# Performance work log

Measured on AMD Instinct MI355X. Metric: run time of the kernel, lower is better.

The kernel has to match this reference:

```python
import jax, jax.numpy as jnp
import numpy as np

N = 8192
IN_DIM = 64
OUT_DIM = 64
HEADS = 2
EPS = 1e-10


def setup_inputs() -> dict:
    key = jax.random.key(0)
    ks = jax.random.split(key, 6)
    features = jax.random.normal(ks[0], (N, IN_DIM), dtype=jnp.float32)
    adj = (jax.random.uniform(ks[1], (N, N)) < 0.005).astype(jnp.float32)
    # per-head attention linear: Linear(2*in_dim, 1) stacked -> [heads, 2*in_dim]
    W_attn = jax.random.normal(ks[2], (HEADS, 2 * IN_DIM), dtype=jnp.float32) * 0.05
    b_attn = jax.random.normal(ks[3], (HEADS,), dtype=jnp.float32) * 0.05
    # feature transform: Linear(in_dim, heads*out_dim)
    W_lin = jax.random.normal(ks[4], (HEADS * OUT_DIM, IN_DIM), dtype=jnp.float32) * 0.05
    b_lin = jax.random.normal(ks[5], (HEADS * OUT_DIM,), dtype=jnp.float32) * 0.05
    return {"adj": adj, "features": features, "W_attn": W_attn,
            "b_attn": b_attn, "W_lin": W_lin, "b_lin": b_lin}


def reference(adj, features, W_attn, b_attn, W_lin, b_lin):
    n, in_dim = features.shape
    heads = W_attn.shape[0]
    # add self-loops (adj + sparse identity in the original)
    idx = jnp.arange(n)
    adj_sl = adj.at[idx, idx].add(1.0)
    # concat-based score: head([x_i ; x_j]) = x_i @ Wa_src + x_j @ Wa_dst + b
    # (avoids the O(N^2 * 2*in_dim) concat tensor the original materializes)
    s_src = features @ W_attn[:, :in_dim].T   # [N, H]
    s_dst = features @ W_attn[:, in_dim:].T   # [N, H]
    # scores[n,h,m] = exp(s_src[n,h] + s_dst[m,h] + b[h])
    scores = jnp.exp(s_src[:, :, None] + s_dst.T[None, :, :] + b_attn[None, :, None])
    scores = scores * adj_sl[:, None, :]                      # adjacency mask
    attn = scores / (jnp.sum(scores, axis=-1, keepdims=True) + EPS)
    # dropout is identity in eval mode (deterministic reference)
    ft = (features @ W_lin.T + b_lin).reshape(n, heads, -1)   # [N, H, OUT]
    out = jnp.einsum('nhm,mhj->nhj', attn, ft)                # aggregate neighbors
    return jax.nn.elu(out.reshape(n, -1))
```

## Files before the change

kernel.cpp:

```cpp
#include <hip/hip_runtime.h>
#include <math.h>

#define NN 8192
#define IN_DIM 64
#define GAT_EPS 1e-10f
#define ECAP 256

typedef float fvec4 __attribute__((ext_vector_type(4)));

__device__ __forceinline__ unsigned nz4(fvec4 v) {
    return (unsigned)(v.x != 0.f) | ((unsigned)(v.y != 0.f) << 1) |
           ((unsigned)(v.z != 0.f) << 2) | ((unsigned)(v.w != 0.f) << 3);
}

__global__ void setup_kernel(const float* __restrict__ features,
                             const float* __restrict__ W_lin,
                             const float* __restrict__ b_lin,
                             const float* __restrict__ W_attn,
                             float2* __restrict__ ftI,
                             float2* __restrict__ pdv) {
    if (blockIdx.x < 2048) {
        int gid = blockIdx.x * blockDim.x + threadIdx.x;
        int n = gid >> 6;
        int c = gid & 63;
        const float4* f4 = (const float4*)(features + (size_t)n * IN_DIM);
        const float4* w0 = (const float4*)(W_lin + (size_t)c * IN_DIM);
        const float4* w1 = (const float4*)(W_lin + (size_t)(64 + c) * IN_DIM);
        float a0 = 0.f, a1 = 0.f;
#pragma unroll
        for (int d = 0; d < IN_DIM / 4; ++d) {
            float4 f = f4[d];
            float4 u = w0[d];
            float4 v = w1[d];
            a0 += f.x * u.x + f.y * u.y + f.z * u.z + f.w * u.w;
            a1 += f.x * v.x + f.y * v.y + f.z * v.z + f.w * v.w;
        }
        ftI[gid] = make_float2(a0 + b_lin[c], a1 + b_lin[64 + c]);
    } else {
        int n = (blockIdx.x - 2048) * blockDim.x + threadIdx.x;
        const float4* f4   = (const float4*)(features + (size_t)n * IN_DIM);
        const float4* wa0d = (const float4*)(W_attn + IN_DIM);
        const float4* wa1d = (const float4*)(W_attn + 3 * IN_DIM);
        float s0 = 0.f, s1 = 0.f;
#pragma unroll
        for (int d = 0; d < IN_DIM / 4; ++d) {
            float4 f = f4[d];
            float4 b = wa0d[d];
            float4 e = wa1d[d];
            s0 += f.x * b.x + f.y * b.y + f.z * b.z + f.w * b.w;
            s1 += f.x * e.x + f.y * e.y + f.z * e.z + f.w * e.w;
        }
        pdv[n] = make_float2(__expf(s0), __expf(s1));
    }
}

__global__ void __launch_bounds__(256) gat_agg_kernel(
        const float* __restrict__ adj,
        const float2* __restrict__ ftI,
        const float2* __restrict__ pdv,
        float* __restrict__ out) {
    __shared__ int edges[4][ECAP];
    __shared__ int ecnt[4];
    int widx = threadIdx.x >> 6;
    int lane = threadIdx.x & 63;
    int n = blockIdx.x * 4 + widx;
    int* ebuf = edges[widx];

    if (lane == 0) ecnt[widx] = 0;

    const fvec4* arow = (const fvec4*)(adj + (size_t)n * NN) + lane;

    fvec4 q[3][4];
#pragma unroll
    for (int r = 0; r < 3; ++r) {
        const fvec4* p = arow + r * 256;
        q[r][0] = __builtin_nontemporal_load(p);
        q[r][1] = __builtin_nontemporal_load(p + 64);
        q[r][2] = __builtin_nontemporal_load(p + 128);
        q[r][3] = __builtin_nontemporal_load(p + 192);
    }

#pragma unroll
    for (int it = 0; it < 8; ++it) {
        int slot = it % 3;
        fvec4 a0 = q[slot][0], a1 = q[slot][1], a2 = q[slot][2], a3 = q[slot][3];
        if (it < 5) {
            const fvec4* p = arow + (it + 3) * 256;
            q[slot][0] = __builtin_nontemporal_load(p);
            q[slot][1] = __builtin_nontemporal_load(p + 64);
            q[slot][2] = __builtin_nontemporal_load(p + 128);
            q[slot][3] = __builtin_nontemporal_load(p + 192);
        }
        unsigned mb = nz4(a0) | (nz4(a1) << 4) | (nz4(a2) << 8) | (nz4(a3) << 12);
        if (mb) {
            int c = __popc(mb);
            int pos = atomicAdd(&ecnt[widx], c);
            int megabase = it * 1024 + lane * 4;
            while (mb) {
                int b = __ffs(mb) - 1;
                mb &= mb - 1;
                ebuf[pos++] = megabase + ((b >> 2) << 8) + (b & 3);
            }
        }
    }

    float2 ps = pdv[n];
    float2 fs = ftI[(size_t)n * 64 + lane];
    float acc0 = ps.x * fs.x, acc1 = ps.y * fs.y;
    float den0 = ps.x, den1 = ps.y;

    __syncthreads();

    int count = ecnt[widx];
    int e = 0;
    for (; e + 8 <= count; e += 8) {
        int4 ma  = *(const int4*)&ebuf[e];
        int4 mbq = *(const int4*)&ebuf[e + 4];
        float2 p0 = pdv[ma.x],  p1 = pdv[ma.y],  p2 = pdv[ma.z],  p3 = pdv[ma.w];
        float2 p4 = pdv[mbq.x], p5 = pdv[mbq.y], p6 = pdv[mbq.z], p7 = pdv[mbq.w];
        float2 f0 = ftI[(size_t)ma.x * 64 + lane];
        float2 f1 = ftI[(size_t)ma.y * 64 + lane];
        float2 f2 = ftI[(size_t)ma.z * 64 + lane];
        float2 f3 = ftI[(size_t)ma.w * 64 + lane];
        float2 f4 = ftI[(size_t)mbq.x * 64 + lane];
        float2 f5 = ftI[(size_t)mbq.y * 64 + lane];
        float2 f6 = ftI[(size_t)mbq.z * 64 + lane];
        float2 f7 = ftI[(size_t)mbq.w * 64 + lane];
        acc0 += p0.x * f0.x + p1.x * f1.x + p2.x * f2.x + p3.x * f3.x
              + p4.x * f4.x + p5.x * f5.x + p6.x * f6.x + p7.x * f7.x;
        acc1 += p0.y * f0.y + p1.y * f1.y + p2.y * f2.y + p3.y * f3.y
              + p4.y * f4.y + p5.y * f5.y + p6.y * f6.y + p7.y * f7.y;
        den0 += p0.x + p1.x + p2.x + p3.x + p4.x + p5.x + p6.x + p7.x;
        den1 += p0.y + p1.y + p2.y + p3.y + p4.y + p5.y + p6.y + p7.y;
    }
    for (; e < count; ++e) {
        int m = ebuf[e];
        float2 p = pdv[m];
        float2 f = ftI[(size_t)m * 64 + lane];
        acc0 += p.x * f.x;
        acc1 += p.y * f.y;
        den0 += p.x;
        den1 += p.y;
    }

    float o0 = acc0 / (den0 + GAT_EPS);
    float o1 = acc1 / (den1 + GAT_EPS);
    o0 = o0 > 0.f ? o0 : expm1f(o0);
    o1 = o1 > 0.f ? o1 : expm1f(o1);
    out[(size_t)n * 128 + lane]      = o0;
    out[(size_t)n * 128 + 64 + lane] = o1;
}

extern "C" void kernel_launch(void* const* d_in, const int* in_sizes, int n_in,
                              void* d_out, int out_size, void* d_ws, size_t ws_size,
                              hipStream_t stream) {
    const float* adj      = (const float*)d_in[0];
    const float* features = (const float*)d_in[1];
    const float* W_attn   = (const float*)d_in[2];
    const float* W_lin    = (const float*)d_in[4];
    const float* b_lin    = (const float*)d_in[5];
    float* out = (float*)d_out;

    float* ws = (float*)d_ws;
    float2* ftI = (float2*)ws;
    float2* pdv = (float2*)(ws + (size_t)NN * 128);

    setup_kernel<<<2048 + 32, 256, 0, stream>>>(features, W_lin, b_lin, W_attn, ftI, pdv);
    gat_agg_kernel<<<NN / 4, 256, 0, stream>>>(adj, ftI, pdv, out);
}
```

Measured before the change: 392.3 us.

## Aggregate raw features first, then apply linear transform per node

```diff
diff --git a/kernel.cpp b/kernel.cpp
--- a/kernel.cpp
+++ b/kernel.cpp
@@ -13,54 +13,35 @@
            ((unsigned)(v.z != 0.f) << 2) | ((unsigned)(v.w != 0.f) << 3);
 }
 
-__global__ void setup_kernel(const float* __restrict__ features,
-                             const float* __restrict__ W_lin,
-                             const float* __restrict__ b_lin,
-                             const float* __restrict__ W_attn,
-                             float2* __restrict__ ftI,
-                             float2* __restrict__ pdv) {
-    if (blockIdx.x < 2048) {
-        int gid = blockIdx.x * blockDim.x + threadIdx.x;
-        int n = gid >> 6;
-        int c = gid & 63;
-        const float4* f4 = (const float4*)(features + (size_t)n * IN_DIM);
-        const float4* w0 = (const float4*)(W_lin + (size_t)c * IN_DIM);
-        const float4* w1 = (const float4*)(W_lin + (size_t)(64 + c) * IN_DIM);
-        float a0 = 0.f, a1 = 0.f;
+__global__ void pdv_kernel(const float* __restrict__ features,
+                           const float* __restrict__ W_attn,
+                           float2* __restrict__ pdv) {
+    int n = blockIdx.x * blockDim.x + threadIdx.x;
+    const float4* f4   = (const float4*)(features + (size_t)n * IN_DIM);
+    const float4* wa0d = (const float4*)(W_attn + IN_DIM);
+    const float4* wa1d = (const float4*)(W_attn + 3 * IN_DIM);
+    float s0 = 0.f, s1 = 0.f;
 #pragma unroll
-        for (int d = 0; d < IN_DIM / 4; ++d) {
-            float4 f = f4[d];
-            float4 u = w0[d];
-            float4 v = w1[d];
-            a0 += f.x * u.x + f.y * u.y + f.z * u.z + f.w * u.w;
-            a1 += f.x * v.x + f.y * v.y + f.z * v.z + f.w * v.w;
-        }
-        ftI[gid] = make_float2(a0 + b_lin[c], a1 + b_lin[64 + c]);
-    } else {
-        int n = (blockIdx.x - 2048) * blockDim.x + threadIdx.x;
-        const float4* f4   = (const float4*)(features + (size_t)n * IN_DIM);
-        const float4* wa0d = (const float4*)(W_attn + IN_DIM);
-        const float4* wa1d = (const float4*)(W_attn + 3 * IN_DIM);
-        float s0 = 0.f, s1 = 0.f;
-#pragma unroll
-        for (int d = 0; d < IN_DIM / 4; ++d) {
-            float4 f = f4[d];
-            float4 b = wa0d[d];
-            float4 e = wa1d[d];
-            s0 += f.x * b.x + f.y * b.y + f.z * b.z + f.w * b.w;
-            s1 += f.x * e.x + f.y * e.y + f.z * e.z + f.w * e.w;
-        }
-        pdv[n] = make_float2(__expf(s0), __expf(s1));
+    for (int d = 0; d < IN_DIM / 4; ++d) {
+        float4 f = f4[d];
+        float4 b = wa0d[d];
+        float4 e = wa1d[d];
+        s0 += f.x * b.x + f.y * b.y + f.z * b.z + f.w * b.w;
+        s1 += f.x * e.x + f.y * e.y + f.z * e.z + f.w * e.w;
     }
+    pdv[n] = make_float2(__expf(s0), __expf(s1));
 }
 
 __global__ void __launch_bounds__(256) gat_agg_kernel(
         const float* __restrict__ adj,
-        const float2* __restrict__ ftI,
+        const float* __restrict__ features,
         const float2* __restrict__ pdv,
+        const float* __restrict__ W_lin,
+        const float* __restrict__ b_lin,
         float* __restrict__ out) {
     __shared__ int edges[4][ECAP];
     __shared__ int ecnt[4];
+    __shared__ float aggbuf[4][2][64];
     int widx = threadIdx.x >> 6;
     int lane = threadIdx.x & 63;
     int n = blockIdx.x * 4 + widx;
@@ -105,8 +86,8 @@
     }
 
     float2 ps = pdv[n];
-    float2 fs = ftI[(size_t)n * 64 + lane];
-    float acc0 = ps.x * fs.x, acc1 = ps.y * fs.y;
+    float fs = features[(size_t)n * 64 + lane];
+    float acc0 = ps.x * fs, acc1 = ps.y * fs;
     float den0 = ps.x, den1 = ps.y;
 
     __syncthreads();
@@ -118,33 +99,51 @@
         int4 mbq = *(const int4*)&ebuf[e + 4];
         float2 p0 = pdv[ma.x],  p1 = pdv[ma.y],  p2 = pdv[ma.z],  p3 = pdv[ma.w];
         float2 p4 = pdv[mbq.x], p5 = pdv[mbq.y], p6 = pdv[mbq.z], p7 = pdv[mbq.w];
-        float2 f0 = ftI[(size_t)ma.x * 64 + lane];
-        float2 f1 = ftI[(size_t)ma.y * 64 + lane];
-        float2 f2 = ftI[(size_t)ma.z * 64 + lane];
-        float2 f3 = ftI[(size_t)ma.w * 64 + lane];
-        float2 f4 = ftI[(size_t)mbq.x * 64 + lane];
-        float2 f5 = ftI[(size_t)mbq.y * 64 + lane];
-        float2 f6 = ftI[(size_t)mbq.z * 64 + lane];
-        float2 f7 = ftI[(size_t)mbq.w * 64 + lane];
-        acc0 += p0.x * f0.x + p1.x * f1.x + p2.x * f2.x + p3.x * f3.x
-              + p4.x * f4.x + p5.x * f5.x + p6.x * f6.x + p7.x * f7.x;
-        acc1 += p0.y * f0.y + p1.y * f1.y + p2.y * f2.y + p3.y * f3.y
-              + p4.y * f4.y + p5.y * f5.y + p6.y * f6.y + p7.y * f7.y;
+        float f0 = features[(size_t)ma.x * 64 + lane];
+        float f1 = features[(size_t)ma.y * 64 + lane];
+        float f2 = features[(size_t)ma.z * 64 + lane];
+        float f3 = features[(size_t)ma.w * 64 + lane];
+        float f4v = features[(size_t)mbq.x * 64 + lane];
+        float f5 = features[(size_t)mbq.y * 64 + lane];
+        float f6 = features[(size_t)mbq.z * 64 + lane];
+        float f7 = features[(size_t)mbq.w * 64 + lane];
+        acc0 += p0.x * f0 + p1.x * f1 + p2.x * f2 + p3.x * f3
+              + p4.x * f4v + p5.x * f5 + p6.x * f6 + p7.x * f7;
+        acc1 += p0.y * f0 + p1.y * f1 + p2.y * f2 + p3.y * f3
+              + p4.y * f4v + p5.y * f5 + p6.y * f6 + p7.y * f7;
         den0 += p0.x + p1.x + p2.x + p3.x + p4.x + p5.x + p6.x + p7.x;
         den1 += p0.y + p1.y + p2.y + p3.y + p4.y + p5.y + p6.y + p7.y;
     }
     for (; e < count; ++e) {
         int m = ebuf[e];
         float2 p = pdv[m];
-        float2 f = ftI[(size_t)m * 64 + lane];
-        acc0 += p.x * f.x;
-        acc1 += p.y * f.y;
+        float f = features[(size_t)m * 64 + lane];
+        acc0 += p.x * f;
+        acc1 += p.y * f;
         den0 += p.x;
         den1 += p.y;
     }
 
-    float o0 = acc0 / (den0 + GAT_EPS);
-    float o1 = acc1 / (den1 + GAT_EPS);
+    aggbuf[widx][0][lane] = acc0 / (den0 + GAT_EPS);
+    aggbuf[widx][1][lane] = acc1 / (den1 + GAT_EPS);
+    __syncthreads();
+
+    const float4* w0 = (const float4*)(W_lin + (size_t)lane * IN_DIM);
+    const float4* w1 = (const float4*)(W_lin + (size_t)(64 + lane) * IN_DIM);
+    const float4* a0p = (const float4*)aggbuf[widx][0];
+    const float4* a1p = (const float4*)aggbuf[widx][1];
+    float o0 = 0.f, o1 = 0.f;
+#pragma unroll
+    for (int d = 0; d < IN_DIM / 4; ++d) {
+        float4 u = w0[d];
+        float4 x = a0p[d];
+        float4 v = w1[d];
+        float4 y = a1p[d];
+        o0 += u.x * x.x + u.y * x.y + u.z * x.z + u.w * x.w;
+        o1 += v.x * y.x + v.y * y.y + v.z * y.z + v.w * y.w;
+    }
+    o0 += b_lin[lane];
+    o1 += b_lin[64 + lane];
     o0 = o0 > 0.f ? o0 : expm1f(o0);
     o1 = o1 > 0.f ? o1 : expm1f(o1);
     out[(size_t)n * 128 + lane]      = o0;
@@ -161,10 +160,8 @@
     const float* b_lin    = (const float*)d_in[5];
     float* out = (float*)d_out;
 
-    float* ws = (float*)d_ws;
-    float2* ftI = (float2*)ws;
-    float2* pdv = (float2*)(ws + (size_t)NN * 128);
+    float2* pdv = (float2*)d_ws;
 
-    setup_kernel<<<2048 + 32, 256, 0, stream>>>(features, W_lin, b_lin, W_attn, ftI, pdv);
-    gat_agg_kernel<<<NN / 4, 256, 0, stream>>>(adj, ftI, pdv, out);
+    pdv_kernel<<<32, 256, 0, stream>>>(features, W_attn, pdv);
+    gat_agg_kernel<<<NN / 4, 256, 0, stream>>>(adj, features, pdv, W_lin, b_lin, out);
 }
```

Result: faster. 374.7 us (-4.5%).
